# Kernel optimization log

Hardware: AMD Instinct MI355X
Metric: run time of the kernel (lower is better)

## Reference

```python
import jax, jax.numpy as jnp
import numpy as np

N_NODES = 100000
N_EDGES = 3200000
IN_DIM = 256
OUT_DIM = 64


def setup_inputs() -> dict:
    key = jax.random.key(0)
    k1, k2, k3 = jax.random.split(key, 3)
    h = jax.random.normal(k1, (N_NODES, IN_DIM), dtype=jnp.float32)
    W = jax.random.normal(k2, (IN_DIM, OUT_DIM), dtype=jnp.float32) * (IN_DIM ** -0.5)
    b = jnp.zeros((OUT_DIM,), dtype=jnp.float32)
    edges = jax.random.randint(k3, (2, N_EDGES), 0, N_NODES, dtype=jnp.int64)
    return {"h": h, "W": W, "b": b, "edges": edges}


def reference(h, W, b, edges):
    # DGL GraphConv, norm='both':
    #   out = D_dst^{-1/2} * A * (D_src^{-1/2} * (h @ W)) + b
    # degrees clamped to min 1; then log_softmax over classes.
    N = h.shape[0]
    src, dst = edges[0], edges[1]
    ones = jnp.ones(src.shape, dtype=h.dtype)
    out_deg = jax.ops.segment_sum(ones, src, num_segments=N)
    in_deg = jax.ops.segment_sum(ones, dst, num_segments=N)
    norm_src = jnp.maximum(out_deg, 1.0) ** -0.5  # [N]
    norm_dst = jnp.maximum(in_deg, 1.0) ** -0.5   # [N]
    # in_dim > out_dim: project first (matches DGL's mult-first optimization)
    m = (h @ W) * norm_src[:, None]               # [N, out_dim]
    agg = jax.ops.segment_sum(m[src], dst, num_segments=N)  # SpMM
    out = agg * norm_dst[:, None] + b
    return jax.nn.log_softmax(out, axis=1)
```

## Files before the change

kernel.cpp:

```cpp
#include <hip/hip_runtime.h>
#include <hip/hip_fp16.h>
#include <math.h>

#define IN_DIM 256
#define OUT_DIM 64
#define BROWS 256
#define HIST_EDGES 8192
#define SC_THREADS 512
#define SC_EPB 16
#define SC_EDGES (SC_THREADS * SC_EPB)
#define BM 128
#define KC 32
#define HS_LD 33

__global__ void __launch_bounds__(256) hist_kernel(
        const int* __restrict__ src, const int* __restrict__ dst,
        int* __restrict__ hist2, int n_edges, int nb) {
    __shared__ int lhd[512];
    __shared__ int lhs[512];
    for (int i = threadIdx.x; i < nb; i += 256) { lhd[i] = 0; lhs[i] = 0; }
    __syncthreads();
    const int base = blockIdx.x * HIST_EDGES;
    for (int i = threadIdx.x; i < HIST_EDGES; i += 256) {
        int e = base + i;
        if (e < n_edges) {
            atomicAdd(&lhd[dst[e] >> 8], 1);
            atomicAdd(&lhs[src[e] >> 8], 1);
        }
    }
    __syncthreads();
    for (int i = threadIdx.x; i < nb; i += 256) {
        if (lhd[i]) atomicAdd(&hist2[i], lhd[i]);
        if (lhs[i]) atomicAdd(&hist2[nb + i], lhs[i]);
    }
}

__global__ void __launch_bounds__(512) scan2_kernel(
        const int* __restrict__ hist2,
        int* __restrict__ dbase, int* __restrict__ dcursor,
        int* __restrict__ sbase, int* __restrict__ scursor,
        int* __restrict__ row_start, int nb, int n_nodes) {
    __shared__ int sc[512];
    const int t = threadIdx.x;
    const int isS = blockIdx.x;
    const int* hsrc = hist2 + (isS ? nb : 0);
    int* base = isS ? sbase : dbase;
    int* cur  = isS ? scursor : dcursor;
    int v = (t < nb) ? hsrc[t] : 0;
    sc[t] = v;
    __syncthreads();
    #pragma unroll
    for (int d = 1; d < 512; d <<= 1) {
        int tv = (t >= d) ? sc[t - d] : 0;
        __syncthreads();
        sc[t] += tv;
        __syncthreads();
    }
    const int excl = sc[t] - v;
    if (t < nb) { base[t] = excl; cur[t] = excl; }
    if (t == nb) {
        base[t] = excl;
        if (!isS) row_start[n_nodes] = excl;
    }
}

__global__ void scan_serial_kernel(const int* __restrict__ hist2,
                                   int* __restrict__ dbase, int* __restrict__ dcursor,
                                   int* __restrict__ sbase, int* __restrict__ scursor,
                                   int* __restrict__ row_start,
                                   int nb, int n_nodes) {
    if (threadIdx.x == 0 && blockIdx.x == 0) {
        int acc = 0;
        for (int i = 0; i < nb; ++i) { dbase[i] = acc; dcursor[i] = acc; acc += hist2[i]; }
        dbase[nb] = acc;
        row_start[n_nodes] = acc;
        acc = 0;
        for (int i = 0; i < nb; ++i) { sbase[i] = acc; scursor[i] = acc; acc += hist2[nb + i]; }
        sbase[nb] = acc;
    }
}

__global__ void __launch_bounds__(SC_THREADS) scatter_pairs_kernel(
        const int* __restrict__ src, const int* __restrict__ dst,
        int* __restrict__ dcursor, int* __restrict__ scursor,
        unsigned* __restrict__ pairs, unsigned char* __restrict__ sbytes,
        int n_edges, int nb) {
    __shared__ int lhd[512];
    __shared__ int lbd[512];
    __shared__ int lhs[512];
    __shared__ int lbs[512];
    const int t = threadIdx.x;
    for (int i = t; i < nb; i += SC_THREADS) { lhd[i] = 0; lhs[i] = 0; }
    __syncthreads();

    const int base = blockIdx.x * SC_EDGES;
    int s[SC_EPB], d[SC_EPB];
    #pragma unroll
    for (int i = 0; i < SC_EPB; ++i) {
        int e = base + i * SC_THREADS + t;
        if (e < n_edges) {
            s[i] = src[e];
            d[i] = dst[e];
            atomicAdd(&lhd[d[i] >> 8], 1);
            atomicAdd(&lhs[s[i] >> 8], 1);
        } else {
            s[i] = -1; d[i] = 0;
        }
    }
    __syncthreads();
    for (int i = t; i < nb; i += SC_THREADS) {
        int c = lhd[i];
        lbd[i] = c ? atomicAdd(&dcursor[i], c) : 0;
        lhd[i] = 0;
        c = lhs[i];
        lbs[i] = c ? atomicAdd(&scursor[i], c) : 0;
        lhs[i] = 0;
    }
    __syncthreads();
    #pragma unroll
    for (int i = 0; i < SC_EPB; ++i) {
        if (s[i] >= 0) {
            int bkt = d[i] >> 8;
            int pos = lbd[bkt] + atomicAdd(&lhd[bkt], 1);
            pairs[pos] = ((unsigned)s[i] << 8) | (unsigned)(d[i] & 255);
            int sb = s[i] >> 8;
            int spos = lbs[sb] + atomicAdd(&lhs[sb], 1);
            sbytes[spos] = (unsigned char)(s[i] & 255);
        }
    }
}

__global__ void __launch_bounds__(256) bucket2csr_kernel(
        const unsigned* __restrict__ pairs, const int* __restrict__ bucket_base,
        int* __restrict__ row_start, int* __restrict__ csr_src, int n_nodes) {
    __shared__ int cnt[BROWS];
    __shared__ int scan[BROWS];
    const int b = blockIdx.x;
    const int beg = bucket_base[b];
    const int end = bucket_base[b + 1];
    const int rowBase = b * BROWS;

    cnt[threadIdx.x] = 0;
    __syncthreads();
    for (int i = beg + threadIdx.x; i < end; i += 256)
        atomicAdd(&cnt[pairs[i] & 255u], 1);
    __syncthreads();

    int v = cnt[threadIdx.x];
    scan[threadIdx.x] = v;
    __syncthreads();
    #pragma unroll
    for (int dstep = 1; dstep < 256; dstep <<= 1) {
        int tv = (threadIdx.x >= dstep) ? scan[threadIdx.x - dstep] : 0;
        __syncthreads();
        scan[threadIdx.x] += tv;
        __syncthreads();
    }
    const int excl = scan[threadIdx.x] - v;

    const int row = rowBase + threadIdx.x;
    if (row < n_nodes) row_start[row] = beg + excl;
    cnt[threadIdx.x] = beg + excl;
    __syncthreads();

    for (int i = beg + threadIdx.x; i < end; i += 256) {
        unsigned p = pairs[i];
        int pos = atomicAdd(&cnt[p & 255u], 1);
        csr_src[pos] = (int)(p >> 8);
    }
}

__global__ void __launch_bounds__(256) count_src_kernel(
        const unsigned char* __restrict__ sbytes, const int* __restrict__ sbase,
        int* __restrict__ out_deg, int n_nodes) {
    __shared__ int cnt[BROWS];
    cnt[threadIdx.x] = 0;
    __syncthreads();
    const int beg = sbase[blockIdx.x];
    const int end = sbase[blockIdx.x + 1];
    for (int i = beg + threadIdx.x; i < end; i += 256)
        atomicAdd(&cnt[sbytes[i]], 1);
    __syncthreads();
    const int row = blockIdx.x * BROWS + threadIdx.x;
    if (row < n_nodes) out_deg[row] = cnt[threadIdx.x];
}

__global__ void __launch_bounds__(256) gemm_kernel(
        const float* __restrict__ h, const float* __restrict__ W,
        const int* __restrict__ out_deg, __half* __restrict__ m, int n_nodes) {
    __shared__ float hs[BM * HS_LD];
    __shared__ float Ws[KC * OUT_DIM];

    const int t = threadIdx.x;
    const int c = t & 15;
    const int g = t >> 4;
    const int rowBase = blockIdx.x * BM;

    float acc[8][4];
    #pragma unroll
    for (int i = 0; i < 8; ++i)
        #pragma unroll
        for (int j = 0; j < 4; ++j) acc[i][j] = 0.f;

    for (int kc = 0; kc < IN_DIM / KC; ++kc) {
        __syncthreads();
        #pragma unroll
        for (int i = 0; i < 4; ++i) {
            int idx = t + 256 * i;
            int row = idx >> 3;
            int seg = idx & 7;
            int grow = rowBase + row;
            float4 v = make_float4(0.f, 0.f, 0.f, 0.f);
            if (grow < n_nodes)
                v = *(const float4*)(h + (size_t)grow * IN_DIM + kc * KC + seg * 4);
            float* dp = &hs[row * HS_LD + seg * 4];
            dp[0] = v.x; dp[1] = v.y; dp[2] = v.z; dp[3] = v.w;
        }
        {
            const float4* Wg = (const float4*)(W + kc * KC * OUT_DIM);
            float4* Wl = (float4*)Ws;
            Wl[t] = Wg[t];
            Wl[t + 256] = Wg[t + 256];
        }
        __syncthreads();

        #pragma unroll 4
        for (int kk = 0; kk < KC; ++kk) {
            float4 bv = *(const float4*)&Ws[kk * OUT_DIM + c * 4];
            #pragma unroll
            for (int i = 0; i < 8; ++i) {
                float a = hs[(g * 8 + i) * HS_LD + kk];
                acc[i][0] += a * bv.x;
                acc[i][1] += a * bv.y;
                acc[i][2] += a * bv.z;
                acc[i][3] += a * bv.w;
            }
        }
    }

    #pragma unroll
    for (int i = 0; i < 8; ++i) {
        int row = rowBase + g * 8 + i;
        if (row < n_nodes) {
            float nr = rsqrtf(fmaxf((float)out_deg[row], 1.0f));
            union { __half2 h2[2]; uint2 u; } pk;
            pk.h2[0] = __floats2half2_rn(acc[i][0] * nr, acc[i][1] * nr);
            pk.h2[1] = __floats2half2_rn(acc[i][2] * nr, acc[i][3] * nr);
            *(uint2*)(m + (size_t)row * OUT_DIM + c * 4) = pk.u;
        }
    }
}

__global__ void __launch_bounds__(256) gather_kernel(
        const int* __restrict__ row_start, const int* __restrict__ csr_src,
        const __half* __restrict__ m, const float* __restrict__ b,
        float* __restrict__ out, int n_nodes) {
    const int wave = threadIdx.x >> 6;
    const int lane = threadIdx.x & 63;
    const int half = lane >> 5;
    const int c    = lane & 31;
    const int row = blockIdx.x * 4 + wave;
    if (row >= n_nodes) return;

    const int beg = row_start[row];
    const int end = row_start[row + 1];
    const __half2* __restrict__ m2 = (const __half2*)m;

    float ax = 0.f, ay = 0.f;
    int i = beg;
    for (; i + 16 <= end; i += 16) {
        int s[8];
        #pragma unroll
        for (int k = 0; k < 8; ++k) s[k] = csr_src[i + 2 * k + half];
        #pragma unroll
        for (int k = 0; k < 8; ++k) {
            float2 f = __half22float2(m2[(unsigned)(s[k] * (OUT_DIM / 2) + c)]);
            ax += f.x; ay += f.y;
        }
    }
    for (int e = i + half; e < end; e += 2) {
        float2 f = __half22float2(m2[(unsigned)(csr_src[e] * (OUT_DIM / 2) + c)]);
        ax += f.x; ay += f.y;
    }
    ax += __shfl_xor(ax, 32, 64);
    ay += __shfl_xor(ay, 32, 64);

    float nd = rsqrtf(fmaxf((float)(end - beg), 1.0f));
    float2 bb = *(const float2*)(b + 2 * c);
    float x0 = ax * nd + bb.x;
    float x1 = ay * nd + bb.y;

    float mx = fmaxf(x0, x1);
    #pragma unroll
    for (int o = 16; o > 0; o >>= 1) mx = fmaxf(mx, __shfl_xor(mx, o, 64));
    float ex0 = expf(x0 - mx), ex1 = expf(x1 - mx);
    float s = ex0 + ex1;
    #pragma unroll
    for (int o = 16; o > 0; o >>= 1) s += __shfl_xor(s, o, 64);
    float ls = logf(s);

    if (half == 0) {
        float2 o2 = make_float2(x0 - mx - ls, x1 - mx - ls);
        *(float2*)(out + (size_t)row * OUT_DIM + 2 * c) = o2;
    }
}

static inline size_t align16(size_t x) { return (x + 15) & ~(size_t)15; }

extern "C" void kernel_launch(void* const* d_in, const int* in_sizes, int n_in,
                              void* d_out, int out_size, void* d_ws, size_t ws_size,
                              hipStream_t stream) {
    const float* h = (const float*)d_in[0];
    const float* W = (const float*)d_in[1];
    const float* b = (const float*)d_in[2];
    const int* edges = (const int*)d_in[3];

    const int out_dim = in_sizes[2];
    const int in_dim  = in_sizes[1] / out_dim;
    const int n_nodes = in_sizes[0] / in_dim;
    const int n_edges = in_sizes[3] / 2;

    const int* src = edges;
    const int* dst = edges + n_edges;

    float* out = (float*)d_out;

    const int nb = (n_nodes + BROWS - 1) / BROWS;

    char* ws = (char*)d_ws;
    size_t off = 0;
    int* out_deg     = (int*)(ws + off); off = align16(off + (size_t)n_nodes * 4);
    int* row_start   = (int*)(ws + off); off = align16(off + (size_t)(n_nodes + 1) * 4);
    int* hist2       = (int*)(ws + off); off = align16(off + (size_t)(2 * nb) * 4);
    int* dbase       = (int*)(ws + off); off = align16(off + (size_t)(nb + 1) * 4);
    int* dcursor     = (int*)(ws + off); off = align16(off + (size_t)nb * 4);
    int* sbase       = (int*)(ws + off); off = align16(off + (size_t)(nb + 1) * 4);
    int* scursor     = (int*)(ws + off); off = align16(off + (size_t)nb * 4);
    __half* m        = (__half*)(ws + off); off = align16(off + (size_t)n_nodes * OUT_DIM * 2);
    unsigned* pairs  = (unsigned*)(ws + off); off = align16(off + (size_t)n_edges * 4);
    int* csr_src     = (int*)(ws + off); off = align16(off + (size_t)n_edges * 4);
    unsigned char* sbytes = (unsigned char*)m;

    (void)hipMemsetAsync(hist2, 0, (size_t)(2 * nb) * sizeof(int), stream);

    const int hist_blocks = (n_edges + HIST_EDGES - 1) / HIST_EDGES;
    const int sc_blocks   = (n_edges + SC_EDGES - 1) / SC_EDGES;

    hist_kernel<<<hist_blocks, 256, 0, stream>>>(src, dst, hist2, n_edges, nb);
    if (nb + 1 <= 512) {
        scan2_kernel<<<2, 512, 0, stream>>>(hist2, dbase, dcursor, sbase, scursor,
                                            row_start, nb, n_nodes);
    } else {
        scan_serial_kernel<<<1, 64, 0, stream>>>(hist2, dbase, dcursor, sbase, scursor,
                                                 row_start, nb, n_nodes);
    }
    scatter_pairs_kernel<<<sc_blocks, SC_THREADS, 0, stream>>>(
        src, dst, dcursor, scursor, pairs, sbytes, n_edges, nb);
    bucket2csr_kernel<<<nb, 256, 0, stream>>>(pairs, dbase, row_start, csr_src, n_nodes);
    count_src_kernel<<<nb, 256, 0, stream>>>(sbytes, sbase, out_deg, n_nodes);

    gemm_kernel<<<(n_nodes + BM - 1) / BM, 256, 0, stream>>>(h, W, out_deg, m, n_nodes);

    gather_kernel<<<(n_nodes + 3) / 4, 256, 0, stream>>>(row_start, csr_src, m, b, out, n_nodes);
}
```

Baseline: 425.9 us.

## Fuse bucket-to-CSR build into gather kernel using LDS-resident CSR per bucket

Removes the separate bucket2csr kernel and global csr_src/row_start arrays. Each 512-thread block now builds its bucket's CSR in shared memory and immediately runs the per-row gather, normalization and log_softmax from it. This saves a global write and read of the edge list and one launch. In exchange, parallelism drops to one block per 256 rows (about 391 blocks) with about 50KB of LDS, which limits occupancy for the latency-bound gather. It also vectorizes the edge loads in the histogram and scatter kernels with int4.

```diff
diff --git a/kernel.cpp b/kernel.cpp
--- a/kernel.cpp
+++ b/kernel.cpp
@@ -12,6 +12,7 @@
 #define BM 128
 #define KC 32
 #define HS_LD 33
+#define CSR_CAP 12288
 
 __global__ void __launch_bounds__(256) hist_kernel(
         const int* __restrict__ src, const int* __restrict__ dst,
@@ -21,11 +22,24 @@
     for (int i = threadIdx.x; i < nb; i += 256) { lhd[i] = 0; lhs[i] = 0; }
     __syncthreads();
     const int base = blockIdx.x * HIST_EDGES;
-    for (int i = threadIdx.x; i < HIST_EDGES; i += 256) {
-        int e = base + i;
-        if (e < n_edges) {
-            atomicAdd(&lhd[dst[e] >> 8], 1);
-            atomicAdd(&lhs[src[e] >> 8], 1);
+    if (base + HIST_EDGES <= n_edges) {
+        const int4* s4 = (const int4*)(src + base);
+        const int4* d4 = (const int4*)(dst + base);
+        for (int i = threadIdx.x; i < HIST_EDGES / 4; i += 256) {
+            int4 a = s4[i];
+            int4 c = d4[i];
+            atomicAdd(&lhs[a.x >> 8], 1); atomicAdd(&lhs[a.y >> 8], 1);
+            atomicAdd(&lhs[a.z >> 8], 1); atomicAdd(&lhs[a.w >> 8], 1);
+            atomicAdd(&lhd[c.x >> 8], 1); atomicAdd(&lhd[c.y >> 8], 1);
+            atomicAdd(&lhd[c.z >> 8], 1); atomicAdd(&lhd[c.w >> 8], 1);
+        }
+    } else {
+        for (int i = threadIdx.x; i < HIST_EDGES; i += 256) {
+            int e = base + i;
+            if (e < n_edges) {
+                atomicAdd(&lhd[dst[e] >> 8], 1);
+                atomicAdd(&lhs[src[e] >> 8], 1);
+            }
         }
     }
     __syncthreads();
@@ -38,8 +52,7 @@
 __global__ void __launch_bounds__(512) scan2_kernel(
         const int* __restrict__ hist2,
         int* __restrict__ dbase, int* __restrict__ dcursor,
-        int* __restrict__ sbase, int* __restrict__ scursor,
-        int* __restrict__ row_start, int nb, int n_nodes) {
+        int* __restrict__ sbase, int* __restrict__ scursor, int nb) {
     __shared__ int sc[512];
     const int t = threadIdx.x;
     const int isS = blockIdx.x;
@@ -58,22 +71,17 @@
     }
     const int excl = sc[t] - v;
     if (t < nb) { base[t] = excl; cur[t] = excl; }
-    if (t == nb) {
-        base[t] = excl;
-        if (!isS) row_start[n_nodes] = excl;
-    }
+    if (t == nb) base[t] = excl;
 }
 
 __global__ void scan_serial_kernel(const int* __restrict__ hist2,
                                    int* __restrict__ dbase, int* __restrict__ dcursor,
                                    int* __restrict__ sbase, int* __restrict__ scursor,
-                                   int* __restrict__ row_start,
-                                   int nb, int n_nodes) {
+                                   int nb) {
     if (threadIdx.x == 0 && blockIdx.x == 0) {
         int acc = 0;
         for (int i = 0; i < nb; ++i) { dbase[i] = acc; dcursor[i] = acc; acc += hist2[i]; }
         dbase[nb] = acc;
-        row_start[n_nodes] = acc;
         acc = 0;
         for (int i = 0; i < nb; ++i) { sbase[i] = acc; scursor[i] = acc; acc += hist2[nb + i]; }
         sbase[nb] = acc;
@@ -95,16 +103,33 @@
 
     const int base = blockIdx.x * SC_EDGES;
     int s[SC_EPB], d[SC_EPB];
-    #pragma unroll
-    for (int i = 0; i < SC_EPB; ++i) {
-        int e = base + i * SC_THREADS + t;
-        if (e < n_edges) {
-            s[i] = src[e];
-            d[i] = dst[e];
+    if (base + SC_EDGES <= n_edges) {
+        const int4* s4 = (const int4*)(src + base);
+        const int4* d4 = (const int4*)(dst + base);
+        #pragma unroll
+        for (int j = 0; j < SC_EPB / 4; ++j) {
+            int4 a = s4[j * SC_THREADS + t];
+            int4 c = d4[j * SC_THREADS + t];
+            s[4*j+0] = a.x; s[4*j+1] = a.y; s[4*j+2] = a.z; s[4*j+3] = a.w;
+            d[4*j+0] = c.x; d[4*j+1] = c.y; d[4*j+2] = c.z; d[4*j+3] = c.w;
+        }
+        #pragma unroll
+        for (int i = 0; i < SC_EPB; ++i) {
             atomicAdd(&lhd[d[i] >> 8], 1);
             atomicAdd(&lhs[s[i] >> 8], 1);
-        } else {
-            s[i] = -1; d[i] = 0;
+        }
+    } else {
+        #pragma unroll
+        for (int i = 0; i < SC_EPB; ++i) {
+            int e = base + i * SC_THREADS + t;
+            if (e < n_edges) {
+                s[i] = src[e];
+                d[i] = dst[e];
+                atomicAdd(&lhd[d[i] >> 8], 1);
+                atomicAdd(&lhs[s[i] >> 8], 1);
+            } else {
+                s[i] = -1; d[i] = 0;
+            }
         }
     }
     __syncthreads();
@@ -127,46 +152,6 @@
             int spos = lbs[sb] + atomicAdd(&lhs[sb], 1);
             sbytes[spos] = (unsigned char)(s[i] & 255);
         }
-    }
-}
-
-__global__ void __launch_bounds__(256) bucket2csr_kernel(
-        const unsigned* __restrict__ pairs, const int* __restrict__ bucket_base,
-        int* __restrict__ row_start, int* __restrict__ csr_src, int n_nodes) {
-    __shared__ int cnt[BROWS];
-    __shared__ int scan[BROWS];
-    const int b = blockIdx.x;
-    const int beg = bucket_base[b];
-    const int end = bucket_base[b + 1];
-    const int rowBase = b * BROWS;
-
-    cnt[threadIdx.x] = 0;
-    __syncthreads();
-    for (int i = beg + threadIdx.x; i < end; i += 256)
-        atomicAdd(&cnt[pairs[i] & 255u], 1);
-    __syncthreads();
-
-    int v = cnt[threadIdx.x];
-    scan[threadIdx.x] = v;
-    __syncthreads();
-    #pragma unroll
-    for (int dstep = 1; dstep < 256; dstep <<= 1) {
-        int tv = (threadIdx.x >= dstep) ? scan[threadIdx.x - dstep] : 0;
-        __syncthreads();
-        scan[threadIdx.x] += tv;
-        __syncthreads();
-    }
-    const int excl = scan[threadIdx.x] - v;
-
-    const int row = rowBase + threadIdx.x;
-    if (row < n_nodes) row_start[row] = beg + excl;
-    cnt[threadIdx.x] = beg + excl;
-    __syncthreads();
-
-    for (int i = beg + threadIdx.x; i < end; i += 256) {
-        unsigned p = pairs[i];
-        int pos = atomicAdd(&cnt[p & 255u], 1);
-        csr_src[pos] = (int)(p >> 8);
     }
 }
 
@@ -251,57 +236,121 @@
     }
 }
 
-__global__ void __launch_bounds__(256) gather_kernel(
-        const int* __restrict__ row_start, const int* __restrict__ csr_src,
+__global__ void __launch_bounds__(512) bucket_gather_kernel(
+        const unsigned* __restrict__ pairs, const int* __restrict__ dbase,
         const __half* __restrict__ m, const float* __restrict__ b,
         float* __restrict__ out, int n_nodes) {
-    const int wave = threadIdx.x >> 6;
-    const int lane = threadIdx.x & 63;
+    __shared__ int cnt[BROWS];
+    __shared__ int rofs[BROWS];
+    __shared__ int cur[BROWS];
+    __shared__ int csr[CSR_CAP];
+
+    const int t = threadIdx.x;
+    const int bkt = blockIdx.x;
+    const int beg = dbase[bkt];
+    const int end = dbase[bkt + 1];
+    const int seg = end - beg;
+    const int rowBase = bkt * BROWS;
+
+    const int wave = t >> 6;
+    const int lane = t & 63;
     const int half = lane >> 5;
     const int c    = lane & 31;
-    const int row = blockIdx.x * 4 + wave;
-    if (row >= n_nodes) return;
-
-    const int beg = row_start[row];
-    const int end = row_start[row + 1];
     const __half2* __restrict__ m2 = (const __half2*)m;
-
-    float ax = 0.f, ay = 0.f;
-    int i = beg;
-    for (; i + 16 <= end; i += 16) {
-        int s[8];
-        #pragma unroll
-        for (int k = 0; k < 8; ++k) s[k] = csr_src[i + 2 * k + half];
-        #pragma unroll
-        for (int k = 0; k < 8; ++k) {
-            float2 f = __half22float2(m2[(unsigned)(s[k] * (OUT_DIM / 2) + c)]);
-            ax += f.x; ay += f.y;
-        }
-    }
-    for (int e = i + half; e < end; e += 2) {
-        float2 f = __half22float2(m2[(unsigned)(csr_src[e] * (OUT_DIM / 2) + c)]);
-        ax += f.x; ay += f.y;
-    }
-    ax += __shfl_xor(ax, 32, 64);
-    ay += __shfl_xor(ay, 32, 64);
-
-    float nd = rsqrtf(fmaxf((float)(end - beg), 1.0f));
-    float2 bb = *(const float2*)(b + 2 * c);
-    float x0 = ax * nd + bb.x;
-    float x1 = ay * nd + bb.y;
-
-    float mx = fmaxf(x0, x1);
-    #pragma unroll
-    for (int o = 16; o > 0; o >>= 1) mx = fmaxf(mx, __shfl_xor(mx, o, 64));
-    float ex0 = expf(x0 - mx), ex1 = expf(x1 - mx);
-    float s = ex0 + ex1;
-    #pragma unroll
-    for (int o = 16; o > 0; o >>= 1) s += __shfl_xor(s, o, 64);
-    float ls = logf(s);
-
-    if (half == 0) {
-        float2 o2 = make_float2(x0 - mx - ls, x1 - mx - ls);
-        *(float2*)(out + (size_t)row * OUT_DIM + 2 * c) = o2;
+    const float2 bb = *(const float2*)(b + 2 * c);
+
+    if (t < BROWS) cnt[t] = 0;
+    __syncthreads();
+
+    if (seg <= CSR_CAP) {
+        for (int i = beg + t; i < end; i += 512)
+            atomicAdd(&cnt[pairs[i] & 255u], 1);
+        __syncthreads();
+        if (t < BROWS) rofs[t] = cnt[t];
+        __syncthreads();
+        #pragma unroll
+        for (int d = 1; d < BROWS; d <<= 1) {
+            int tv = (t < BROWS && t >= d) ? rofs[t - d] : 0;
+            __syncthreads();
+            if (t < BROWS) rofs[t] += tv;
+            __syncthreads();
+        }
+        if (t < BROWS) cur[t] = rofs[t] - cnt[t];
+        __syncthreads();
+        for (int i = beg + t; i < end; i += 512) {
+            unsigned p = pairs[i];
+            int pos = atomicAdd(&cur[p & 255u], 1);
+            csr[pos] = (int)(p >> 8);
+        }
+        __syncthreads();
+        for (int r = wave; r < BROWS; r += 8) {
+            const int row = rowBase + r;
+            if (row >= n_nodes) continue;
+            const int cend = rofs[r];
+            const int cbeg = cend - cnt[r];
+            float ax = 0.f, ay = 0.f;
+            int i = cbeg;
+            for (; i + 16 <= cend; i += 16) {
+                int s[8];
+                #pragma unroll
+                for (int k = 0; k < 8; ++k) s[k] = csr[i + 2 * k + half];
+                #pragma unroll
+                for (int k = 0; k < 8; ++k) {
+                    float2 f = __half22float2(m2[(unsigned)(s[k] * (OUT_DIM / 2) + c)]);
+                    ax += f.x; ay += f.y;
+                }
+            }
+            for (int e = i + half; e < cend; e += 2) {
+                float2 f = __half22float2(m2[(unsigned)(csr[e] * (OUT_DIM / 2) + c)]);
+                ax += f.x; ay += f.y;
+            }
+            ax += __shfl_xor(ax, 32, 64);
+            ay += __shfl_xor(ay, 32, 64);
+
+            float nd = rsqrtf(fmaxf((float)cnt[r], 1.0f));
+            float x0 = ax * nd + bb.x;
+            float x1 = ay * nd + bb.y;
+            float mx = fmaxf(x0, x1);
+            #pragma unroll
+            for (int o = 16; o > 0; o >>= 1) mx = fmaxf(mx, __shfl_xor(mx, o, 64));
+            float ex0 = expf(x0 - mx), ex1 = expf(x1 - mx);
+            float sm = ex0 + ex1;
+            #pragma unroll
+            for (int o = 16; o > 0; o >>= 1) sm += __shfl_xor(sm, o, 64);
+            float ls = logf(sm);
+            if (half == 0)
+                *(float2*)(out + (size_t)row * OUT_DIM + 2 * c) =
+                    make_float2(x0 - mx - ls, x1 - mx - ls);
+        }
+    } else {
+        for (int r = wave; r < BROWS; r += 8) {
+            const int row = rowBase + r;
+            if (row >= n_nodes) continue;
+            float ax = 0.f, ay = 0.f;
+            int deg = 0;
+            for (int e = beg; e < end; ++e) {
+                unsigned p = pairs[e];
+                if ((int)(p & 255u) == r) {
+                    ++deg;
+                    float2 f = __half22float2(m2[(unsigned)((p >> 8) * (OUT_DIM / 2) + c)]);
+                    ax += f.x; ay += f.y;
+                }
+            }
+            float nd = rsqrtf(fmaxf((float)deg, 1.0f));
+            float x0 = ax * nd + bb.x;
+            float x1 = ay * nd + bb.y;
+            float mx = fmaxf(x0, x1);
+            #pragma unroll
+            for (int o = 16; o > 0; o >>= 1) mx = fmaxf(mx, __shfl_xor(mx, o, 64));
+            float ex0 = expf(x0 - mx), ex1 = expf(x1 - mx);
+            float sm = ex0 + ex1;
+            #pragma unroll
+            for (int o = 16; o > 0; o >>= 1) sm += __shfl_xor(sm, o, 64);
+            float ls = logf(sm);
+            if (half == 0)
+                *(float2*)(out + (size_t)row * OUT_DIM + 2 * c) =
+                    make_float2(x0 - mx - ls, x1 - mx - ls);
+        }
     }
 }
 
@@ -330,7 +379,6 @@
     char* ws = (char*)d_ws;
     size_t off = 0;
     int* out_deg     = (int*)(ws + off); off = align16(off + (size_t)n_nodes * 4);
-    int* row_start   = (int*)(ws + off); off = align16(off + (size_t)(n_nodes + 1) * 4);
     int* hist2       = (int*)(ws + off); off = align16(off + (size_t)(2 * nb) * 4);
     int* dbase       = (int*)(ws + off); off = align16(off + (size_t)(nb + 1) * 4);
     int* dcursor     = (int*)(ws + off); off = align16(off + (size_t)nb * 4);
@@ -338,7 +386,6 @@
     int* scursor     = (int*)(ws + off); off = align16(off + (size_t)nb * 4);
     __half* m        = (__half*)(ws + off); off = align16(off + (size_t)n_nodes * OUT_DIM * 2);
     unsigned* pairs  = (unsigned*)(ws + off); off = align16(off + (size_t)n_edges * 4);
-    int* csr_src     = (int*)(ws + off); off = align16(off + (size_t)n_edges * 4);
     unsigned char* sbytes = (unsigned char*)m;
 
     (void)hipMemsetAsync(hist2, 0, (size_t)(2 * nb) * sizeof(int), stream);
@@ -348,18 +395,15 @@
 
     hist_kernel<<<hist_blocks, 256, 0, stream>>>(src, dst, hist2, n_edges, nb);
     if (nb + 1 <= 512) {
-        scan2_kernel<<<2, 512, 0, stream>>>(hist2, dbase, dcursor, sbase, scursor,
-                                            row_start, nb, n_nodes);
+        scan2_kernel<<<2, 512, 0, stream>>>(hist2, dbase, dcursor, sbase, scursor, nb);
     } else {
-        scan_serial_kernel<<<1, 64, 0, stream>>>(hist2, dbase, dcursor, sbase, scursor,
-                                                 row_start, nb, n_nodes);
+        scan_serial_kernel<<<1, 64, 0, stream>>>(hist2, dbase, dcursor, sbase, scursor, nb);
     }
     scatter_pairs_kernel<<<sc_blocks, SC_THREADS, 0, stream>>>(
         src, dst, dcursor, scursor, pairs, sbytes, n_edges, nb);
-    bucket2csr_kernel<<<nb, 256, 0, stream>>>(pairs, dbase, row_start, csr_src, n_nodes);
     count_src_kernel<<<nb, 256, 0, stream>>>(sbytes, sbase, out_deg, n_nodes);
 
     gemm_kernel<<<(n_nodes + BM - 1) / BM, 256, 0, stream>>>(h, W, out_deg, m, n_nodes);
 
-    gather_kernel<<<(n_nodes + 3) / 4, 256, 0, stream>>>(row_start, csr_src, m, b, out, n_nodes);
-}
+    bucket_gather_kernel<<<nb, 512, 0, stream>>>(pairs, dbase, m, b, out, n_nodes);
+}
```

New measurement: 405.3 us. -4.9%, faster.
